# Optimization experiments

Hardware: AMD Instinct MI355X
Metric: run time of the kernel (lower is better)

The kernel has to match this reference:

```python
import jax, jax.numpy as jnp
import numpy as np

B, S, D = 256, 512, 128
H1, H2 = 256, 512


def setup_inputs() -> dict:
    key = jax.random.key(0)
    ks = jax.random.split(key, 13)
    s = lambda k, shape, scale=0.05: jax.random.normal(k, shape, dtype=jnp.float32) * scale
    return {
        "x": jax.random.normal(ks[0], (B, S, D), dtype=jnp.float32),
        "conv_w": s(ks[1], (H1, D)),
        "conv_b": s(ks[2], (H1,)),
        "w_ih": s(ks[3], (4 * H2, H1)),
        "b_ih": s(ks[4], (4 * H2,)),
        "w_hh": s(ks[5], (4 * H2, H2)),
        "b_hh": s(ks[6], (4 * H2,)),
        "h0": s(ks[7], (B, H2)),
        "c0": s(ks[8], (B, H2)),
        "fc1_w": s(ks[9], (H2, H2)),
        "fc1_b": s(ks[10], (H2,)),
        "fc2_w": s(ks[11], (1, H2)),
        "fc2_b": s(ks[12], (1,)),
    }


def reference(x, conv_w, conv_b, w_ih, b_ih, w_hh, b_hh, h0, c0,
              fc1_w, fc1_b, fc2_w, fc2_b):
    # Conv1d with kernel_size=1 == pointwise linear over feature dim
    embed = jnp.einsum('bsd,hd->bsh', x, conv_w) + conv_b  # [B,S,H1]

    def step(carry, e_t):
        h, c = carry
        # PyTorch LSTMCell: gates in order i, f, g, o
        gates = e_t @ w_ih.T + b_ih + h @ w_hh.T + b_hh  # [B,4H2]
        i, f, g, o = jnp.split(gates, 4, axis=-1)
        i = jax.nn.sigmoid(i)
        f = jax.nn.sigmoid(f)
        g = jnp.tanh(g)
        o = jax.nn.sigmoid(o)
        c = f * c + i * g
        h = o * jnp.tanh(c)
        return (h, c), h

    _, hs = jax.lax.scan(step, (h0, c0), jnp.swapaxes(embed, 0, 1))  # hs: [S,B,H2]
    pooled = hs.sum(axis=0)  # sum over sequence -> [B,H2]
    dec = jax.nn.relu(pooled @ fc1_w.T + fc1_b)
    v = (dec @ fc2_w.T + fc2_b).squeeze(-1)  # [B]
    return v
```

## Files before the change

### kernel.cpp

```cpp
#include <hip/hip_runtime.h>
#include <hip/hip_cooperative_groups.h>


typedef __attribute__((ext_vector_type(8))) short s16x8;
typedef __attribute__((ext_vector_type(4))) float f32x4;

#define B_   256
#define S_   512
#define D_   128
#define H1_  256
#define H2_  512
#define G4_  2048
#define K_   640

__device__ __forceinline__ unsigned short f2bf(float f) {
  union { float f; unsigned u; } v; v.f = f;
  unsigned r = v.u + 0x7FFFu + ((v.u >> 16) & 1u);
  return (unsigned short)(r >> 16);
}
__device__ __forceinline__ float sigm(float x) { return 1.f / (1.f + __expf(-x)); }
__device__ __forceinline__ float tanh_(float x) { return 1.f - 2.f / (__expf(2.f * x) + 1.f); }

__device__ __forceinline__ s16x8 ld_cohx8(const unsigned short* p) {
  s16x8 d;
  asm volatile("global_load_dwordx4 %0, %1, off sc0 sc1" : "=v"(d) : "v"(p));
  return d;
}
__device__ __forceinline__ void st_coh_u16(unsigned short* p, unsigned v) {
  asm volatile("global_store_short %0, %1, off sc0 sc1" :: "v"(p), "v"(v) : "memory");
}
__device__ __forceinline__ void st_coh_u32(unsigned* p, unsigned v) {
  asm volatile("global_store_dword %0, %1, off sc0 sc1" :: "v"(p), "v"(v) : "memory");
}
__device__ __forceinline__ unsigned ld_coh_u32(const unsigned* p) {
  unsigned d;
  asm volatile("global_load_dword %0, %1, off sc0 sc1\n\ts_waitcnt vmcnt(0)"
               : "=v"(d) : "v"(p) : "memory");
  return d;
}
__device__ __forceinline__ void vm_drain() {
  asm volatile("s_waitcnt vmcnt(0)" ::: "memory");
  __builtin_amdgcn_sched_barrier(0);
}

__global__ void prep_kernel(const float* __restrict__ conv_w, const float* __restrict__ conv_b,
                            const float* __restrict__ w_ih,   const float* __restrict__ b_ih,
                            const float* __restrict__ w_hh,   const float* __restrict__ b_hh,
                            unsigned short* __restrict__ Wc,  float* __restrict__ bias,
                            unsigned* __restrict__ flags) {
  const int np = blockIdx.x;
  const int g = np & 3, j = np >> 2;
  const int n = g * H2_ + j;
  const int tid = threadIdx.x;

  if (np == 0) { flags[tid] = 0; flags[tid + 128] = 0; }

  __shared__ float wrow[H1_];
  __shared__ float red[128];
  wrow[tid]       = w_ih[(size_t)n * H1_ + tid];
  wrow[tid + 128] = w_ih[(size_t)n * H1_ + tid + 128];
  __syncthreads();

  float acc = 0.f;
  for (int h1 = 0; h1 < H1_; ++h1)
    acc += wrow[h1] * conv_w[(size_t)h1 * D_ + tid];
  Wc[(size_t)np * K_ + tid] = f2bf(acc);

  #pragma unroll
  for (int r = 0; r < 4; ++r)
    Wc[(size_t)np * K_ + 128 + tid + r * 128] = f2bf(w_hh[(size_t)n * H2_ + tid + r * 128]);

  float p = wrow[tid] * conv_b[tid] + wrow[tid + 128] * conv_b[tid + 128];
  red[tid] = p;
  __syncthreads();
  for (int s = 64; s > 0; s >>= 1) {
    if (tid < s) red[tid] += red[tid + s];
    __syncthreads();
  }
  if (tid == 0) bias[np] = red[0] + b_ih[n] + b_hh[n];
}

__global__ __launch_bounds__(256, 1) void lstm_kernel(
    const float* __restrict__ x, const float* __restrict__ h0,
    const float* __restrict__ c0, const unsigned short* __restrict__ Wc,
    const float* __restrict__ bias, unsigned short* __restrict__ h_bf,
    float* __restrict__ pooled, unsigned* __restrict__ flags) {
  const int wg = blockIdx.x;
  const int mg = wg & 15;
  const int ng = wg >> 4;
  const int tid = threadIdx.x;
  const int wv = tid >> 6;
  const int lane = tid & 63;

  __shared__ unsigned short Alds[16 * K_];

  const int n0 = ng * 128 + wv * 32;
  s16x8 bfrag0[20], bfrag1[20];
  {
    const int bn0 = n0 + (lane & 15);
    const int bk = (lane >> 4) * 8;
    #pragma unroll
    for (int kk = 0; kk < 20; ++kk) {
      bfrag0[kk] = *(const s16x8*)(Wc + (size_t)bn0 * K_ + kk * 32 + bk);
      bfrag1[kk] = *(const s16x8*)(Wc + (size_t)(bn0 + 16) * K_ + kk * 32 + bk);
    }
  }
  #pragma unroll
  for (int kk = 0; kk < 20; ++kk)
    asm volatile("" : "+v"(bfrag0[kk]), "+v"(bfrag1[kk]));

  const int b_own = mg * 16 + (lane & 15);
  const int j0 = ng * 32 + wv * 8 + (lane >> 4);
  const int j1 = j0 + 4;
  const f32x4 brg0 = *(const f32x4*)(bias + 4 * j0);
  const f32x4 brg1 = *(const f32x4*)(bias + 4 * j1);
  float cA = c0[(size_t)b_own * H2_ + j0];
  float cB = c0[(size_t)b_own * H2_ + j1];
  float poolA = 0.f, poolB = 0.f;

  const int sr = tid >> 4, sct = tid & 15;
  const int b_st = mg * 16 + sr;
  const unsigned row_base = sr * (K_ * 2);
  const unsigned swz = (unsigned)((sr & 7) << 4);
  const unsigned swz_x = (row_base + sct * 16) ^ swz;

  const int ar = lane & 15;
  const int ahi = lane >> 4;
  unsigned* fgrp = flags + mg * 16;

  {
    const float* xp = x + ((size_t)b_st * S_) * D_ + sct * 8;
    f32x4 v0 = *(const f32x4*)xp;
    f32x4 v1 = *(const f32x4*)(xp + 4);
    s16x8 pk;
    pk[0] = (short)f2bf(v0[0]); pk[1] = (short)f2bf(v0[1]);
    pk[2] = (short)f2bf(v0[2]); pk[3] = (short)f2bf(v0[3]);
    pk[4] = (short)f2bf(v1[0]); pk[5] = (short)f2bf(v1[1]);
    pk[6] = (short)f2bf(v1[2]); pk[7] = (short)f2bf(v1[3]);
    *(s16x8*)((char*)Alds + swz_x) = pk;
  }

  #pragma unroll 1
  for (int t = 0; t < S_; ++t) {
    unsigned short* hout = h_bf + ((t + 1) & 1) * (B_ * H2_);

    if (t == 0) {
      const float* hp = h0 + (size_t)b_st * H2_ + sct * 32;
      #pragma unroll
      for (int q = 0; q < 4; ++q) {
        f32x4 a = *(const f32x4*)(hp + q * 8);
        f32x4 b = *(const f32x4*)(hp + q * 8 + 4);
        s16x8 pk;
        pk[0] = (short)f2bf(a[0]); pk[1] = (short)f2bf(a[1]);
        pk[2] = (short)f2bf(a[2]); pk[3] = (short)f2bf(a[3]);
        pk[4] = (short)f2bf(b[0]); pk[5] = (short)f2bf(b[1]);
        pk[6] = (short)f2bf(b[2]); pk[7] = (short)f2bf(b[3]);
        unsigned byte = row_base + 256 + sct * 64 + q * 16;
        *(s16x8*)((char*)Alds + (byte ^ swz)) = pk;
      }
    } else {
      const unsigned short* hin = h_bf + (t & 1) * (B_ * H2_);
      const unsigned short* hrow = hin + (size_t)b_st * H2_ + sct * 32;
      s16x8 hv0 = ld_cohx8(hrow);
      s16x8 hv1 = ld_cohx8(hrow + 8);
      s16x8 hv2 = ld_cohx8(hrow + 16);
      s16x8 hv3 = ld_cohx8(hrow + 24);
      vm_drain();
      unsigned byte = row_base + 256 + sct * 64;
      *(s16x8*)((char*)Alds + ((byte     ) ^ swz)) = hv0;
      *(s16x8*)((char*)Alds + ((byte + 16) ^ swz)) = hv1;
      *(s16x8*)((char*)Alds + ((byte + 32) ^ swz)) = hv2;
      *(s16x8*)((char*)Alds + ((byte + 48) ^ swz)) = hv3;
    }
    f32x4 vx0, vx1;
    if (t < S_ - 1) {
      const float* xp = x + ((size_t)b_st * S_ + (t + 1)) * D_ + sct * 8;
      vx0 = *(const f32x4*)xp;
      vx1 = *(const f32x4*)(xp + 4);
    }
    __syncthreads();

    f32x4 acc0 = {0.f, 0.f, 0.f, 0.f};
    f32x4 acc1 = {0.f, 0.f, 0.f, 0.f};
    #pragma unroll
    for (int kk = 0; kk < 20; ++kk) {
      unsigned byte = (unsigned)(ar * (K_ * 2) + kk * 64 + ahi * 16);
      s16x8 af = *(const s16x8*)((const char*)Alds + (byte ^ ((ar & 7) << 4)));
      acc0 = __builtin_amdgcn_mfma_f32_16x16x32_bf16(bfrag0[kk], af, acc0, 0, 0, 0);
      acc1 = __builtin_amdgcn_mfma_f32_16x16x32_bf16(bfrag1[kk], af, acc1, 0, 0, 0);
    }

    {
      float iA = sigm(acc0[0] + brg0[0]);
      float fA = sigm(acc0[1] + brg0[1]);
      float gA = tanh_(acc0[2] + brg0[2]);
      float oA = sigm(acc0[3] + brg0[3]);
      cA = fA * cA + iA * gA;
      float hA = oA * tanh_(cA);
      poolA += hA;
      float iB = sigm(acc1[0] + brg1[0]);
      float fB = sigm(acc1[1] + brg1[1]);
      float gB = tanh_(acc1[2] + brg1[2]);
      float oB = sigm(acc1[3] + brg1[3]);
      cB = fB * cB + iB * gB;
      float hB = oB * tanh_(cB);
      poolB += hB;
      if (t < S_ - 1) {
        st_coh_u16(hout + (size_t)b_own * H2_ + j0, (unsigned)f2bf(hA));
        st_coh_u16(hout + (size_t)b_own * H2_ + j1, (unsigned)f2bf(hB));
      }
    }

    if (t < S_ - 1) {
      vm_drain();
      __syncthreads();
      if (tid == 0) st_coh_u32(fgrp + ng, (unsigned)(t + 1));

      {
        s16x8 pk;
        pk[0] = (short)f2bf(vx0[0]); pk[1] = (short)f2bf(vx0[1]);
        pk[2] = (short)f2bf(vx0[2]); pk[3] = (short)f2bf(vx0[3]);
        pk[4] = (short)f2bf(vx1[0]); pk[5] = (short)f2bf(vx1[1]);
        pk[6] = (short)f2bf(vx1[2]); pk[7] = (short)f2bf(vx1[3]);
        *(s16x8*)((char*)Alds + swz_x) = pk;
      }

      const unsigned tgt = (unsigned)(t + 1);
      const unsigned* fp = fgrp + (lane & 15);
      while (!__all(ld_coh_u32(fp) >= tgt))
        __builtin_amdgcn_s_sleep(1);
    }
  }

  pooled[(size_t)b_own * H2_ + j0] = poolA;
  pooled[(size_t)b_own * H2_ + j1] = poolB;
}

__global__ void fc_kernel(const float* __restrict__ pooled,
                          const float* __restrict__ fc1_w, const float* __restrict__ fc1_b,
                          const float* __restrict__ fc2_w, const float* __restrict__ fc2_b,
                          float* __restrict__ out) {
  const int b = blockIdx.x;
  const int tid = threadIdx.x;
  __shared__ float prow[H2_];
  __shared__ float dec[H2_];
  __shared__ float red[256];
  prow[tid]       = pooled[(size_t)b * H2_ + tid];
  prow[tid + 256] = pooled[(size_t)b * H2_ + tid + 256];
  __syncthreads();
  #pragma unroll
  for (int e = 0; e < 2; ++e) {
    const int o = tid + e * 256;
    const float* wrow = fc1_w + (size_t)o * H2_;
    float a = fc1_b[o];
    #pragma unroll 8
    for (int k = 0; k < H2_; ++k) a += prow[k] * wrow[k];
    dec[o] = fmaxf(a, 0.f);
  }
  __syncthreads();
  red[tid] = dec[tid] * fc2_w[tid] + dec[tid + 256] * fc2_w[tid + 256];
  __syncthreads();
  for (int s = 128; s > 0; s >>= 1) {
    if (tid < s) red[tid] += red[tid + s];
    __syncthreads();
  }
  if (tid == 0) out[b] = red[0] + fc2_b[0];
}

extern "C" void kernel_launch(void* const* d_in, const int* in_sizes, int n_in,
                              void* d_out, int out_size, void* d_ws, size_t ws_size,
                              hipStream_t stream) {
  const float* x      = (const float*)d_in[0];
  const float* conv_w = (const float*)d_in[1];
  const float* conv_b = (const float*)d_in[2];
  const float* w_ih   = (const float*)d_in[3];
  const float* b_ih   = (const float*)d_in[4];
  const float* w_hh   = (const float*)d_in[5];
  const float* b_hh   = (const float*)d_in[6];
  const float* h0     = (const float*)d_in[7];
  const float* c0     = (const float*)d_in[8];
  const float* fc1_w  = (const float*)d_in[9];
  const float* fc1_b  = (const float*)d_in[10];
  const float* fc2_w  = (const float*)d_in[11];
  const float* fc2_b  = (const float*)d_in[12];
  float* out = (float*)d_out;

  char* ws = (char*)d_ws;
  unsigned short* Wc    = (unsigned short*)(ws);
  float* bias           = (float*)(ws + 2621440);
  unsigned short* h_bf  = (unsigned short*)(ws + 2629632);
  float* pooled         = (float*)(ws + 3153920);
  unsigned* flags       = (unsigned*)(ws + 3678208);

  prep_kernel<<<dim3(G4_), dim3(128), 0, stream>>>(conv_w, conv_b, w_ih, b_ih,
                                                   w_hh, b_hh, Wc, bias, flags);

  void* args[8];
  args[0] = (void*)&x;    args[1] = (void*)&h0;   args[2] = (void*)&c0;
  args[3] = (void*)&Wc;   args[4] = (void*)&bias; args[5] = (void*)&h_bf;
  args[6] = (void*)&pooled; args[7] = (void*)&flags;
  hipLaunchCooperativeKernel((void*)lstm_kernel, dim3(256), dim3(256), args, 0, stream);

  fc_kernel<<<dim3(B_), dim3(256), 0, stream>>>(pooled, fc1_w, fc1_b, fc2_w, fc2_b, out);
}
```

Baseline: 1.914 ms.

## Permute weight rows so each lane owns adjacent hidden units and packs stores

Reorders the fused weight and bias rows in the prep kernel so each lane's two MFMA output columns map to adjacent hidden indices j0 and j0+1. This lets each lane write its two bf16 h values as one packed 32-bit coherent store instead of two 16-bit stores. It also uses vectorized c0 loads and pooled writes. The x bf16 packing is moved ahead of the vm drain and barrier to shorten the serialized section between steps. It depends on the permutation staying consistent between the prep and LSTM kernels.

```diff
diff --git a/kernel.cpp b/kernel.cpp
--- a/kernel.cpp
+++ b/kernel.cpp
@@ -4,6 +4,7 @@
 
 typedef __attribute__((ext_vector_type(8))) short s16x8;
 typedef __attribute__((ext_vector_type(4))) float f32x4;
+typedef __attribute__((ext_vector_type(2))) float f32x2;
 
 #define B_   256
 #define S_   512
@@ -26,9 +27,6 @@
   asm volatile("global_load_dwordx4 %0, %1, off sc0 sc1" : "=v"(d) : "v"(p));
   return d;
 }
-__device__ __forceinline__ void st_coh_u16(unsigned short* p, unsigned v) {
-  asm volatile("global_store_short %0, %1, off sc0 sc1" :: "v"(p), "v"(v) : "memory");
-}
 __device__ __forceinline__ void st_coh_u32(unsigned* p, unsigned v) {
   asm volatile("global_store_dword %0, %1, off sc0 sc1" :: "v"(p), "v"(v) : "memory");
 }
@@ -49,7 +47,9 @@
                             unsigned short* __restrict__ Wc,  float* __restrict__ bias,
                             unsigned* __restrict__ flags) {
   const int np = blockIdx.x;
-  const int g = np & 3, j = np >> 2;
+  const int c = np >> 5, r5 = np & 31;
+  const int blk = r5 >> 4, q = (r5 >> 2) & 3, g = r5 & 3;
+  const int j = c * 8 + 2 * q + blk;
   const int n = g * H2_ + j;
   const int tid = threadIdx.x;
 
@@ -77,7 +77,7 @@
     if (tid < s) red[tid] += red[tid + s];
     __syncthreads();
   }
-  if (tid == 0) bias[np] = red[0] + b_ih[n] + b_hh[n];
+  if (tid == 0) bias[4 * j + g] = red[0] + b_ih[n] + b_hh[n];
 }
 
 __global__ __launch_bounds__(256, 1) void lstm_kernel(
@@ -110,13 +110,11 @@
     asm volatile("" : "+v"(bfrag0[kk]), "+v"(bfrag1[kk]));
 
   const int b_own = mg * 16 + (lane & 15);
-  const int j0 = ng * 32 + wv * 8 + (lane >> 4);
-  const int j1 = j0 + 4;
+  const int j0 = ng * 32 + wv * 8 + 2 * (lane >> 4);
   const f32x4 brg0 = *(const f32x4*)(bias + 4 * j0);
-  const f32x4 brg1 = *(const f32x4*)(bias + 4 * j1);
-  float cA = c0[(size_t)b_own * H2_ + j0];
-  float cB = c0[(size_t)b_own * H2_ + j1];
-  float poolA = 0.f, poolB = 0.f;
+  const f32x4 brg1 = *(const f32x4*)(bias + 4 * (j0 + 1));
+  f32x2 c_reg = *(const f32x2*)(c0 + (size_t)b_own * H2_ + j0);
+  f32x2 pool_acc = {0.f, 0.f};
 
   const int sr = tid >> 4, sct = tid & 15;
   const int b_st = mg * 16 + sr;
@@ -195,35 +193,34 @@
       float fA = sigm(acc0[1] + brg0[1]);
       float gA = tanh_(acc0[2] + brg0[2]);
       float oA = sigm(acc0[3] + brg0[3]);
-      cA = fA * cA + iA * gA;
-      float hA = oA * tanh_(cA);
-      poolA += hA;
+      c_reg[0] = fA * c_reg[0] + iA * gA;
+      float hA = oA * tanh_(c_reg[0]);
+      pool_acc[0] += hA;
       float iB = sigm(acc1[0] + brg1[0]);
       float fB = sigm(acc1[1] + brg1[1]);
       float gB = tanh_(acc1[2] + brg1[2]);
       float oB = sigm(acc1[3] + brg1[3]);
-      cB = fB * cB + iB * gB;
-      float hB = oB * tanh_(cB);
-      poolB += hB;
+      c_reg[1] = fB * c_reg[1] + iB * gB;
+      float hB = oB * tanh_(c_reg[1]);
+      pool_acc[1] += hB;
       if (t < S_ - 1) {
-        st_coh_u16(hout + (size_t)b_own * H2_ + j0, (unsigned)f2bf(hA));
-        st_coh_u16(hout + (size_t)b_own * H2_ + j1, (unsigned)f2bf(hB));
+        unsigned packed = (unsigned)f2bf(hA) | ((unsigned)f2bf(hB) << 16);
+        st_coh_u32((unsigned*)(hout + (size_t)b_own * H2_ + j0), packed);
       }
     }
 
     if (t < S_ - 1) {
+      s16x8 pk;
+      pk[0] = (short)f2bf(vx0[0]); pk[1] = (short)f2bf(vx0[1]);
+      pk[2] = (short)f2bf(vx0[2]); pk[3] = (short)f2bf(vx0[3]);
+      pk[4] = (short)f2bf(vx1[0]); pk[5] = (short)f2bf(vx1[1]);
+      pk[6] = (short)f2bf(vx1[2]); pk[7] = (short)f2bf(vx1[3]);
+
       vm_drain();
       __syncthreads();
       if (tid == 0) st_coh_u32(fgrp + ng, (unsigned)(t + 1));
 
-      {
-        s16x8 pk;
-        pk[0] = (short)f2bf(vx0[0]); pk[1] = (short)f2bf(vx0[1]);
-        pk[2] = (short)f2bf(vx0[2]); pk[3] = (short)f2bf(vx0[3]);
-        pk[4] = (short)f2bf(vx1[0]); pk[5] = (short)f2bf(vx1[1]);
-        pk[6] = (short)f2bf(vx1[2]); pk[7] = (short)f2bf(vx1[3]);
-        *(s16x8*)((char*)Alds + swz_x) = pk;
-      }
+      *(s16x8*)((char*)Alds + swz_x) = pk;
 
       const unsigned tgt = (unsigned)(t + 1);
       const unsigned* fp = fgrp + (lane & 15);
@@ -232,8 +229,7 @@
     }
   }
 
-  pooled[(size_t)b_own * H2_ + j0] = poolA;
-  pooled[(size_t)b_own * H2_ + j1] = poolB;
+  *(f32x2*)(pooled + (size_t)b_own * H2_ + j0) = pool_acc;
 }
 
 __global__ void fc_kernel(const float* __restrict__ pooled,
```

Result: faster. 1.784 ms (-6.8%).
